# Performance work log

Hardware: AMD Instinct MI355X
Metric: run time of the kernel (lower is better)

Reference implementation:

```python
import jax, jax.numpy as jnp
import numpy as np
from functools import partial

B, N, U, E, OUT = 32, 1024, 32, 64, 64   # batch, nodes, gru units, embed dim, output dim
LIT, SEM = 12, 16                         # literal / semantic feature dims
T_FWD, L_MLP = 5, 2                       # CFGForwardTime, MLPLayer


def _gru_seq(seq, Wk, Wr, b):
    """Keras GRU (reset_after=True), return full sequence. seq: [B,T,F]."""
    b_in, b_rec = b[0], b[1]
    xproj = jnp.einsum('btf,fu->btu', seq, Wk) + b_in          # [B,T,3U]
    h0 = jnp.zeros((seq.shape[0], U), seq.dtype)

    def step(h, xt):
        rec = h @ Wr + b_rec
        xz, xr, xh = jnp.split(xt, 3, axis=-1)
        rz, rr, rh = jnp.split(rec, 3, axis=-1)
        z = jax.nn.sigmoid(xz + rz)
        r = jax.nn.sigmoid(xr + rr)
        hh = jnp.tanh(xh + r * rh)
        hn = z * h + (1.0 - z) * hh
        return hn, hn

    _, ys = jax.lax.scan(step, h0, jnp.transpose(xproj, (1, 0, 2)))
    return jnp.transpose(ys, (1, 0, 2))                         # [B,T,U]


def _data_layer(lit, sem, Win, bin_, Wout, bout, gk, grk, gb):
    mid = jax.nn.relu(lit @ Win + bin_)            # [B,N,E]
    literal = jax.nn.relu(mid @ Wout + bout)       # [B,N,32]
    semantic = _gru_seq(sem, gk, grk, gb)          # [B,N,32]
    return jnp.concatenate([literal, semantic], axis=-1)  # [B,N,64]


def _graph_layer(inp, cfg, mlpW, mlpb, wOut, bOut):
    e = jax.nn.relu(inp)
    for _ in range(T_FWD):
        t = jnp.einsum('bnm,bmd->bnd', cfg, e)     # message passing
        for i in range(L_MLP):
            t = jax.nn.relu(t @ mlpW[i] + mlpb[i])
        e = jnp.tanh(e + t)
    mid = jnp.sum(e, axis=1)                       # [B,E]
    return mid @ wOut + bOut                       # [B,OUT]


def _cosine(a, b):
    an = a / jnp.sqrt(jnp.maximum(jnp.sum(a * a, -1, keepdims=True), 1e-12))
    bn = b / jnp.sqrt(jnp.maximum(jnp.sum(b * b, -1, keepdims=True), 1e-12))
    return -jnp.sum(an * bn, -1)                   # keras cosine_similarity = -cos


def setup_inputs():
    key = jax.random.key(0)
    ks = jax.random.split(key, 32)
    g = lambda i, shp, s=0.05: jax.random.normal(ks[i], shp, jnp.float32) * s
    inp = {
        'CFG1ST': jax.random.randint(ks[0], (B, N, N), 0, 2, jnp.int32),
        'PFG1ST': jnp.zeros((1,), jnp.float32),
        'LITERAL1ST': jax.random.normal(ks[1], (B, N, LIT), jnp.float32),
        'SEMANTIC1ST': jax.random.normal(ks[2], (B, N, SEM), jnp.float32),
        'CFG2ND': jax.random.randint(ks[3], (B, N, N), 0, 2, jnp.int32),
        'PFG2ND': jnp.zeros((1,), jnp.float32),
        'LITERAL2ND': jax.random.normal(ks[4], (B, N, LIT), jnp.float32),
        'SEMANTIC2ND': jax.random.normal(ks[5], (B, N, SEM), jnp.float32),
        # data layer 1 params
        'd1_Win': g(6, (LIT, E)), 'd1_bin': jnp.zeros((E,), jnp.float32),
        'd1_Wout': g(7, (E, U)), 'd1_bout': jnp.zeros((U,), jnp.float32),
        'd1_gk': g(8, (SEM, 3 * U)), 'd1_grk': g(9, (U, 3 * U)),
        'd1_gb': jnp.zeros((2, 3 * U), jnp.float32),
        # data layer 2 params
        'd2_Win': g(10, (LIT, E)), 'd2_bin': jnp.zeros((E,), jnp.float32),
        'd2_Wout': g(11, (E, U)), 'd2_bout': jnp.zeros((U,), jnp.float32),
        'd2_gk': g(12, (SEM, 3 * U)), 'd2_grk': g(13, (U, 3 * U)),
        'd2_gb': jnp.zeros((2, 3 * U), jnp.float32),
        # shared graph layer params
        'mlpW': g(14, (L_MLP, E, E)), 'mlpb': jnp.zeros((L_MLP, E), jnp.float32),
        'wOut': g(15, (E, OUT)), 'bOut': jnp.zeros((OUT,), jnp.float32),
    }
    return inp


def reference(CFG1ST, PFG1ST, LITERAL1ST, SEMANTIC1ST, CFG2ND, PFG2ND, LITERAL2ND, SEMANTIC2ND,
              d1_Win, d1_bin, d1_Wout, d1_bout, d1_gk, d1_grk, d1_gb,
              d2_Win, d2_bin, d2_Wout, d2_bout, d2_gk, d2_grk, d2_gb,
              mlpW, mlpb, wOut, bOut):
    bb1 = _data_layer(LITERAL1ST, SEMANTIC1ST, d1_Win, d1_bin, d1_Wout, d1_bout, d1_gk, d1_grk, d1_gb)
    e1 = _graph_layer(bb1, CFG1ST.astype(jnp.float32), mlpW, mlpb, wOut, bOut)
    bb2 = _data_layer(LITERAL2ND, SEMANTIC2ND, d2_Win, d2_bin, d2_Wout, d2_bout, d2_gk, d2_grk, d2_gb)
    e2 = _graph_layer(bb2, CFG2ND.astype(jnp.float32), mlpW, mlpb, wOut, bOut)
    cosin = _cosine(e1, e2)
    label = -(cosin - 1.0) / 2.0
    return label  # [B]
```

## Files before the change

kernel.cpp:

```cpp
#include <hip/hip_runtime.h>
#include <stdint.h>
#include <math.h>

#define B_   32
#define N_   1024
#define U_   32
#define E_   64
#define LIT_ 12
#define SEM_ 16
#define GBN  64

typedef float f32x4 __attribute__((ext_vector_type(4)));
typedef short s16x8 __attribute__((ext_vector_type(8)));
#define MFMA_BF16(a,b,c) __builtin_amdgcn_mfma_f32_16x16x32_bf16(a,b,c,0,0,0)

#define F_ET0H 0ULL
#define F_ET0L 8388608ULL
#define F_ET1H 16777216ULL
#define F_ET1L 25165824ULL
#define F_EBUF 33554432ULL
#define F_CFGB 50331648ULL
#define F_WBUF 58720256ULL
#define F_MIN  58753024ULL

#define O_XPROJ 0ULL
#define O_T     25165824ULL
#define O_E     41943040ULL
#define O_OW    58720256ULL
#define O_MIN   58736640ULL

__device__ __forceinline__ float rdlane(float v, int k) {
    return __int_as_float(__builtin_amdgcn_readlane(__float_as_int(v), k));
}
__device__ __forceinline__ unsigned short bf16rne(float x) {
    unsigned u = __float_as_uint(x);
    return (unsigned short)((u + 0x7FFFu + ((u >> 16) & 1u)) >> 16);
}
__device__ __forceinline__ void hilo(float x, short& h, short& l) {
    unsigned short hb = bf16rne(x);
    float hf = __uint_as_float(((unsigned)hb) << 16);
    h = (short)hb;
    l = (short)bf16rne(x - hf);
}

__global__ __launch_bounds__(64) void k_pre(
    const float* __restrict__ lit1, const float* __restrict__ sem1,
    const float* __restrict__ lit2, const float* __restrict__ sem2,
    const float* __restrict__ Win1, const float* __restrict__ bin1,
    const float* __restrict__ Wout1, const float* __restrict__ bout1,
    const float* __restrict__ gk1, const float* __restrict__ gb1,
    const float* __restrict__ Win2, const float* __restrict__ bin2,
    const float* __restrict__ Wout2, const float* __restrict__ bout2,
    const float* __restrict__ gk2, const float* __restrict__ gb2,
    float* __restrict__ ebuf, float* __restrict__ xproj,
    const int* __restrict__ c1, const int* __restrict__ c2,
    uint8_t* __restrict__ cfgb,
    const float* __restrict__ mlpW, short* __restrict__ wbuf)
{
    const int tid = threadIdx.x;
    if (blockIdx.x >= 8192) {
        if (blockIdx.x <= 12287) {
            int g = blockIdx.x - 8192;
            long long gt = (long long)g * 64 + tid;
            #pragma unroll 4
            for (int it = 0; it < 32; ++it) {
                long long o = gt + 262144LL * it;
                const int* src = (o < 4194304LL) ? c1 : c2;
                long long oo = (o < 4194304LL) ? o : o - 4194304LL;
                const int4* p = (const int4*)(src + oo * 8);
                int4 v0 = p[0], v1 = p[1];
                unsigned bb = (unsigned)(v0.x & 1) | ((unsigned)(v0.y & 1) << 1) |
                              ((unsigned)(v0.z & 1) << 2) | ((unsigned)(v0.w & 1) << 3) |
                              ((unsigned)(v1.x & 1) << 4) | ((unsigned)(v1.y & 1) << 5) |
                              ((unsigned)(v1.z & 1) << 6) | ((unsigned)(v1.w & 1) << 7);
                cfgb[o] = (uint8_t)bb;
            }
        } else {
            for (int idx = tid; idx < 8192; idx += 64) {
                int layer = idx >> 12, rem = idx & 4095, out = rem >> 6, in = rem & 63;
                float x = mlpW[layer * 4096 + in * 64 + out];
                short h, l2; hilo(x, h, l2);
                wbuf[layer * 8192 + out * 64 + in] = h;
                wbuf[layer * 8192 + 4096 + out * 64 + in] = l2;
            }
        }
        return;
    }

    __shared__ float lit_ls[LIT_];
    __shared__ float sem_ls[SEM_];
    __shared__ float mid_ls[E_];
    const long long rowbase = (long long)blockIdx.x * 8;
    for (int rr = 0; rr < 8; ++rr) {
        long long row = rowbase + rr;
        int g = (int)(row >> 15);
        long long nIdx = row & 32767;
        const float* lit  = g ? lit2  : lit1;
        const float* sem  = g ? sem2  : sem1;
        const float* Win  = g ? Win2  : Win1;
        const float* bin  = g ? bin2  : bin1;
        const float* Wout = g ? Wout2 : Wout1;
        const float* bout = g ? bout2 : bout1;
        const float* gk   = g ? gk2   : gk1;
        const float* gbp  = g ? gb2   : gb1;

        if (tid < LIT_) lit_ls[tid] = lit[nIdx * LIT_ + tid];
        if (tid < SEM_) sem_ls[tid] = sem[nIdx * SEM_ + tid];
        __syncthreads();

        float acc = bin[tid];
        #pragma unroll
        for (int k = 0; k < LIT_; ++k) acc += lit_ls[k] * Win[k * E_ + tid];
        mid_ls[tid] = fmaxf(acc, 0.f);
        __syncthreads();

        if (tid < U_) {
            float a = bout[tid];
            #pragma unroll
            for (int k = 0; k < E_; ++k) a += mid_ls[k] * Wout[k * U_ + tid];
            ebuf[row * E_ + tid] = fmaxf(a, 0.f);
        }
        {
            float a = gbp[tid];
            #pragma unroll
            for (int k = 0; k < SEM_; ++k) a += sem_ls[k] * gk[k * 96 + tid];
            xproj[row * 96 + tid] = a;
        }
        if (tid < 32) {
            int c = 64 + tid;
            float a2 = gbp[c];
            #pragma unroll
            for (int k = 0; k < SEM_; ++k) a2 += sem_ls[k] * gk[k * 96 + c];
            xproj[row * 96 + c] = a2;
        }
        __syncthreads();
    }
}

__global__ __launch_bounds__(64) void k_gru(
    const float* __restrict__ grk1, const float* __restrict__ gb1,
    const float* __restrict__ grk2, const float* __restrict__ gb2,
    const float* __restrict__ xproj, float* __restrict__ ebuf)
{
    const int gb_i = blockIdx.x;
    const int g = gb_i >> 5;
    const float* grk = g ? grk2 : grk1;
    const float* gbp = g ? gb2 : gb1;
    const int l = threadIdx.x;
    const int j = l & 31;

    float wzr[32];
    float wh[32];
    #pragma unroll
    for (int k = 0; k < 32; ++k) {
        wzr[k] = grk[k * 96 + l];
        wh[k]  = grk[k * 96 + 64 + j];
    }
    const float brec0 = gbp[96 + l];
    const float brec1 = gbp[96 + 64 + j];

    const float* xp = xproj + (long long)gb_i * N_ * 96;
    float* eb = ebuf + (long long)gb_i * N_ * E_ + 32;

    float h = 0.f;

    auto STEP = [&](float X0, float X1, int T) {
        float a0 = brec0, a1 = 0.f, a2 = 0.f, a3 = 0.f;
        float b0 = brec1, b1 = 0.f, b2 = 0.f, b3 = 0.f;
        #pragma unroll
        for (int k = 0; k < 32; k += 4) {
            float h0 = rdlane(h, k);
            float h1 = rdlane(h, k + 1);
            float h2 = rdlane(h, k + 2);
            float h3 = rdlane(h, k + 3);
            a0 = fmaf(h0, wzr[k],     a0);  b0 = fmaf(h0, wh[k],     b0);
            a1 = fmaf(h1, wzr[k + 1], a1);  b1 = fmaf(h1, wh[k + 1], b1);
            a2 = fmaf(h2, wzr[k + 2], a2);  b2 = fmaf(h2, wh[k + 2], b2);
            a3 = fmaf(h3, wzr[k + 3], a3);  b3 = fmaf(h3, wh[k + 3], b3);
        }
        float rec0 = (a0 + a1) + (a2 + a3);
        float rec1 = (b0 + b1) + (b2 + b3);
        float s = 1.f / (1.f + __expf(-(X0 + rec0)));
        float zv = __shfl(s, j);
        float rv = __shfl(s, j + 32);
        float y  = X1 + rv * rec1;
        float e2 = __expf(2.f * y);
        float hh = 1.f - 2.f / (e2 + 1.f);
        float hn = hh + zv * (h - hh);
        h = hn;
        if (l < 32) eb[(long long)(T) * E_ + l] = fmaxf(hn, 0.f);
    };

    float x0a = xp[l],       x1a = xp[64 + j];
    float x0b = xp[96 + l],  x1b = xp[96 + 64 + j];

    for (int t = 0; t < N_; t += 2) {
        float nx0a = xp[(long long)(t + 2) * 96 + l];
        float nx1a = xp[(long long)(t + 2) * 96 + 64 + j];
        float nx0b = xp[(long long)(t + 3) * 96 + l];
        float nx1b = xp[(long long)(t + 3) * 96 + 64 + j];
        STEP(x0a, x1a, t);
        STEP(x0b, x1b, t + 1);
        x0a = nx0a; x1a = nx1a; x0b = nx0b; x1b = nx1b;
    }
}

__global__ __launch_bounds__(256) void k_etr(const float* __restrict__ ebuf,
                                             short* __restrict__ eTh)
{
    __shared__ float tls[128][68];
    const int blk = blockIdx.x, gb = blk >> 3, n0 = (blk & 7) * 128;
    const int tid = threadIdx.x;
    const float4* src = (const float4*)(ebuf + ((size_t)gb * N_ + n0) * E_);
    #pragma unroll
    for (int i = 0; i < 8; ++i) {
        int idx = tid + 256 * i;
        float4 v = src[idx];
        int row = idx >> 4, c4 = (idx & 15) << 2;
        tls[row][c4] = v.x; tls[row][c4 + 1] = v.y;
        tls[row][c4 + 2] = v.z; tls[row][c4 + 3] = v.w;
    }
    __syncthreads();
    const int w = tid >> 6, l = tid & 63;
    short* dh = eTh + ((size_t)gb << 16) + (size_t)l * 1024 + n0 + w * 32;
    #pragma unroll
    for (int ch = 0; ch < 4; ++ch) {
        s16x8 vh;
        #pragma unroll
        for (int i = 0; i < 8; ++i)
            vh[i] = (short)bf16rne(tls[w * 32 + ch * 8 + i][l]);
        *(s16x8*)(dh + ch * 8) = vh;
    }
}

template<int WET>
__global__ __launch_bounds__(256, 2) void k_msgmlp(
    const uint8_t* __restrict__ cfgb,
    const short* __restrict__ eThS, short* __restrict__ eThD,
    float* __restrict__ ebuf,
    const short* __restrict__ wbuf, const float* __restrict__ mlpb)
{
    __shared__ float tls[128][68];
    __shared__ __align__(8) unsigned lut16[32];
    __shared__ uint32_t cls[128][36];
    const int blk = blockIdx.x, gb = blk >> 3, n0 = (blk & 7) * 128;
    const int tid = threadIdx.x, w = tid >> 6, l = tid & 63;
    const int lr = l & 15, lk8 = (l >> 4) * 8;

    if (tid < 32) {
        unsigned e = tid >> 1, hf = tid & 1;
        unsigned b0 = (e >> (2 * hf)) & 1u, b1 = (e >> (2 * hf + 1)) & 1u;
        lut16[tid] = (b0 ? 0x3F80u : 0u) | (b1 ? 0x3F800000u : 0u);
    }
    {
        const uint4* srcv = (const uint4*)(cfgb + ((size_t)gb << 17) + (size_t)n0 * 128);
        #pragma unroll
        for (int i = 0; i < 4; ++i) {
            int idx = tid + 256 * i;
            uint4 v = srcv[idx];
            int base = idx * 4;
            int row = base >> 5, col = base & 31;
            *(uint4*)&cls[row][col] = v;
        }
    }
    __syncthreads();

    const short* bh = eThS + ((size_t)gb << 16) + (size_t)(w * 16 + lr) * 1024 + lk8;

    f32x4 acc[8];
    #pragma unroll
    for (int rt = 0; rt < 8; ++rt) acc[rt] = (f32x4){0.f, 0.f, 0.f, 0.f};

    #pragma unroll 2
    for (int kk = 0; kk < 1024; kk += 32) {
        s16x8 vh = *(const s16x8*)(bh + kk);
        #pragma unroll
        for (int rt = 0; rt < 8; ++rt) {
            unsigned dw = cls[rt * 16 + lr][kk >> 5];
            unsigned nb0 = (dw >> lk8) & 0xFu;
            unsigned nb1 = (dw >> (lk8 + 4)) & 0xFu;
            union { s16x8 v; unsigned long long d[2]; } A;
            A.d[0] = *(const unsigned long long*)&lut16[nb0 * 2];
            A.d[1] = *(const unsigned long long*)&lut16[nb1 * 2];
            acc[rt] = MFMA_BF16(A.v, vh, acc[rt]);
        }
    }

    #pragma unroll
    for (int rt = 0; rt < 8; ++rt)
        #pragma unroll
        for (int r = 0; r < 4; ++r)
            tls[rt * 16 + (l >> 4) * 4 + r][w * 16 + lr] = acc[rt][r];
    __syncthreads();

    float b0c[4], b1c[4];
    #pragma unroll
    for (int nt = 0; nt < 4; ++nt) {
        b0c[nt] = mlpb[nt * 16 + lr];
        b1c[nt] = mlpb[64 + nt * 16 + lr];
    }

    s16x8 ah[2][2], al[2][2];
    #pragma unroll
    for (int mt = 0; mt < 2; ++mt)
        #pragma unroll
        for (int kt = 0; kt < 2; ++kt) {
            const float* p = &tls[w * 32 + mt * 16 + lr][kt * 32 + lk8];
            #pragma unroll
            for (int i = 0; i < 8; ++i) { short hh, ll; hilo(p[i], hh, ll); ah[mt][kt][i] = hh; al[mt][kt][i] = ll; }
        }
    {
        f32x4 acc1[2][4];
        #pragma unroll
        for (int mt = 0; mt < 2; ++mt)
            #pragma unroll
            for (int nt = 0; nt < 4; ++nt)
                acc1[mt][nt] = (f32x4){b0c[nt], b0c[nt], b0c[nt], b0c[nt]};
        #pragma unroll
        for (int nt = 0; nt < 4; ++nt)
            #pragma unroll
            for (int kt = 0; kt < 2; ++kt) {
                s16x8 wth = *(const s16x8*)(wbuf + (nt * 16 + lr) * 64 + kt * 32 + lk8);
                s16x8 wtl = *(const s16x8*)(wbuf + 4096 + (nt * 16 + lr) * 64 + kt * 32 + lk8);
                #pragma unroll
                for (int mt = 0; mt < 2; ++mt) {
                    acc1[mt][nt] = MFMA_BF16(ah[mt][kt], wth, acc1[mt][nt]);
                    acc1[mt][nt] = MFMA_BF16(ah[mt][kt], wtl, acc1[mt][nt]);
                    acc1[mt][nt] = MFMA_BF16(al[mt][kt], wth, acc1[mt][nt]);
                }
            }
        #pragma unroll
        for (int mt = 0; mt < 2; ++mt)
            #pragma unroll
            for (int nt = 0; nt < 4; ++nt)
                #pragma unroll
                for (int r = 0; r < 4; ++r)
                    tls[w * 32 + mt * 16 + (l >> 4) * 4 + r][nt * 16 + lr] = fmaxf(acc1[mt][nt][r], 0.f);
    }

    #pragma unroll
    for (int mt = 0; mt < 2; ++mt)
        #pragma unroll
        for (int kt = 0; kt < 2; ++kt) {
            const float* p = &tls[w * 32 + mt * 16 + lr][kt * 32 + lk8];
            #pragma unroll
            for (int i = 0; i < 8; ++i) { short hh, ll; hilo(p[i], hh, ll); ah[mt][kt][i] = hh; al[mt][kt][i] = ll; }
        }
    f32x4 acc2[2][4];
    #pragma unroll
    for (int mt = 0; mt < 2; ++mt)
        #pragma unroll
        for (int nt = 0; nt < 4; ++nt)
            acc2[mt][nt] = (f32x4){b1c[nt], b1c[nt], b1c[nt], b1c[nt]};
    #pragma unroll
    for (int nt = 0; nt < 4; ++nt)
        #pragma unroll
        for (int kt = 0; kt < 2; ++kt) {
            s16x8 wth = *(const s16x8*)(wbuf + 8192 + (nt * 16 + lr) * 64 + kt * 32 + lk8);
            s16x8 wtl = *(const s16x8*)(wbuf + 8192 + 4096 + (nt * 16 + lr) * 64 + kt * 32 + lk8);
            #pragma unroll
            for (int mt = 0; mt < 2; ++mt) {
                acc2[mt][nt] = MFMA_BF16(ah[mt][kt], wth, acc2[mt][nt]);
                acc2[mt][nt] = MFMA_BF16(ah[mt][kt], wtl, acc2[mt][nt]);
                acc2[mt][nt] = MFMA_BF16(al[mt][kt], wth, acc2[mt][nt]);
            }
        }

    float* eb = ebuf + ((size_t)gb * N_ + n0) * E_;
    #pragma unroll
    for (int mt = 0; mt < 2; ++mt)
        #pragma unroll
        for (int nt = 0; nt < 4; ++nt)
            #pragma unroll
            for (int r = 0; r < 4; ++r) {
                int row = w * 32 + mt * 16 + (l >> 4) * 4 + r;
                int colq = nt * 16 + lr;
                float t2 = fmaxf(acc2[mt][nt][r], 0.f);
                float y = eb[(size_t)row * E_ + colq] + t2;
                float e2 = __expf(2.f * y);
                float en = 1.f - 2.f / (e2 + 1.f);
                eb[(size_t)row * E_ + colq] = en;
                if (WET) tls[row][colq] = en;
            }

    if (WET) {
        short* dh = eThD + ((size_t)gb << 16) + (size_t)l * 1024 + n0 + w * 32;
        #pragma unroll
        for (int ch = 0; ch < 4; ++ch) {
            s16x8 vh;
            #pragma unroll
            for (int i = 0; i < 8; ++i)
                vh[i] = (short)bf16rne(tls[w * 32 + ch * 8 + i][l]);
            *(s16x8*)(dh + ch * 8) = vh;
        }
    }
}

__global__ __launch_bounds__(256) void k_outp(const float* __restrict__ ebuf,
                                              float* __restrict__ part)
{
    const int gb = blockIdx.x >> 2, ch = blockIdx.x & 3;
    const int col = threadIdx.x & 63, r0 = threadIdx.x >> 6;
    const float* eb = ebuf + ((size_t)gb * N_ + ch * 256) * E_;
    float s = 0.f;
    #pragma unroll 8
    for (int i = 0; i < 64; ++i) s += eb[(size_t)(r0 + i * 4) * E_ + col];
    __shared__ float sm[4][64];
    sm[r0][col] = s;
    __syncthreads();
    if (threadIdx.x < 64)
        part[(gb * 4 + ch) * 64 + threadIdx.x] =
            sm[0][threadIdx.x] + sm[1][threadIdx.x] + sm[2][threadIdx.x] + sm[3][threadIdx.x];
}

__global__ __launch_bounds__(64) void k_fin(const float* __restrict__ part,
                                            const float* __restrict__ wOut,
                                            const float* __restrict__ bOut,
                                            float* __restrict__ dout)
{
    const int b = blockIdx.x, d = threadIdx.x;
    __shared__ float m1[64], m2[64];
    m1[d] = part[(b * 4 + 0) * 64 + d] + part[(b * 4 + 1) * 64 + d] +
            part[(b * 4 + 2) * 64 + d] + part[(b * 4 + 3) * 64 + d];
    m2[d] = part[((32 + b) * 4 + 0) * 64 + d] + part[((32 + b) * 4 + 1) * 64 + d] +
            part[((32 + b) * 4 + 2) * 64 + d] + part[((32 + b) * 4 + 3) * 64 + d];
    __syncthreads();
// ... 194 lines not shown
    }
}

extern "C" void kernel_launch(void* const* d_in, const int* in_sizes, int n_in,
                              void* d_out, int out_size, void* d_ws, size_t ws_size,
                              hipStream_t stream) {
    const int*   CFG1 = (const int*)d_in[0];
    const float* LIT1 = (const float*)d_in[2];
    const float* SEM1 = (const float*)d_in[3];
    const int*   CFG2 = (const int*)d_in[4];
    const float* LIT2 = (const float*)d_in[6];
    const float* SEM2 = (const float*)d_in[7];
    const float* d1_Win  = (const float*)d_in[8];
    const float* d1_bin  = (const float*)d_in[9];
    const float* d1_Wout = (const float*)d_in[10];
    const float* d1_bout = (const float*)d_in[11];
    const float* d1_gk   = (const float*)d_in[12];
    const float* d1_grk  = (const float*)d_in[13];
    const float* d1_gb   = (const float*)d_in[14];
    const float* d2_Win  = (const float*)d_in[15];
    const float* d2_bin  = (const float*)d_in[16];
    const float* d2_Wout = (const float*)d_in[17];
    const float* d2_bout = (const float*)d_in[18];
    const float* d2_gk   = (const float*)d_in[19];
    const float* d2_grk  = (const float*)d_in[20];
    const float* d2_gb   = (const float*)d_in[21];
    const float* mlpW = (const float*)d_in[22];
    const float* mlpb = (const float*)d_in[23];
    const float* wOut = (const float*)d_in[24];
    const float* bOut = (const float*)d_in[25];

    char* ws = (char*)d_ws;

    if (ws_size >= F_MIN) {
        float*   xproj = (float*)(ws + 0);
        short*   eT0h  = (short*)(ws + F_ET0H);
        short*   eT1h  = (short*)(ws + F_ET1H);
        float*   ebuf  = (float*)(ws + F_EBUF);
        uint8_t* cfgb  = (uint8_t*)(ws + F_CFGB);
        short*   wbuf  = (short*)(ws + F_WBUF);
        float*   part  = (float*)(ws + F_ET1L);

        k_pre<<<12289, 64, 0, stream>>>(LIT1, SEM1, LIT2, SEM2,
                                        d1_Win, d1_bin, d1_Wout, d1_bout, d1_gk, d1_gb,
                                        d2_Win, d2_bin, d2_Wout, d2_bout, d2_gk, d2_gb,
                                        ebuf, xproj, CFG1, CFG2, cfgb, mlpW, wbuf);

        k_gru<<<64, 64, 0, stream>>>(d1_grk, d1_gb, d2_grk, d2_gb, xproj, ebuf);

        k_etr<<<512, 256, 0, stream>>>(ebuf, eT0h);

        for (int it = 0; it < 5; ++it) {
            short* sh = (it & 1) ? eT1h : eT0h;
            short* dh = (it & 1) ? eT0h : eT1h;
            if (it < 4)
                k_msgmlp<1><<<512, 256, 0, stream>>>(cfgb, sh, dh, ebuf, wbuf, mlpb);
            else
                k_msgmlp<0><<<512, 256, 0, stream>>>(cfgb, sh, dh, ebuf, wbuf, mlpb);
        }

        k_outp<<<256, 256, 0, stream>>>(ebuf, part);
        k_fin<<<32, 64, 0, stream>>>(part, wOut, bOut, (float*)d_out);
    } else if (ws_size >= O_MIN) {
        float* xproj = (float*)(ws + O_XPROJ);
        float* tbuf  = (float*)(ws + O_T);
        float* ebuf  = (float*)(ws + O_E);
        float* outws = (float*)(ws + O_OW);

        k_pre<<<8192, 64, 0, stream>>>(LIT1, SEM1, LIT2, SEM2,
                                       d1_Win, d1_bin, d1_Wout, d1_bout, d1_gk, d1_gb,
                                       d2_Win, d2_bin, d2_Wout, d2_bout, d2_gk, d2_gb,
                                       ebuf, xproj, CFG1, CFG2, (uint8_t*)ws, mlpW, (short*)ws);

        k_gru<<<64, 64, 0, stream>>>(d1_grk, d1_gb, d2_grk, d2_gb, xproj, ebuf);

        for (int it = 0; it < 5; ++it) {
            k_msg_fb<<<512, 256, 0, stream>>>(CFG1, CFG2, ebuf, tbuf);
            k_mlp_fb<<<1024, 64, 0, stream>>>(tbuf, ebuf, mlpW, mlpb);
        }

        k_out<<<GBN, 64, 0, stream>>>(ebuf, wOut, bOut, outws);
        k_cos<<<32, 64, 0, stream>>>(outws, (float*)d_out);
    }
}
```

Measured before the change: 716.3 us.

## Pack two GRU sequences per wave and retile message-passing MFMA loop

The GRU kernel now runs two sequences per 64-lane wave, one per half. Each lane computes its z, r and h gate dot products directly, broadcasting h with ds_swizzle instead of readlane and dropping the cross-lane shuffle, so half as many blocks are launched. The message-passing kernel builds the 0/1 bf16 A fragment from the bitmask with bit arithmetic instead of an LDS lookup table. Each wave now covers 32 rows against all 64 feature columns, with 4 B loads per k step, and the sync after the accumulator store is removed. The serial GRU chain per lane does more FMAs per step. The removed __syncthreads may be a race unless later code is per-wave only.

```diff
diff --git a/kernel.cpp b/kernel.cpp
--- a/kernel.cpp
+++ b/kernel.cpp
@@ -15,7 +15,6 @@
 #define MFMA_BF16(a,b,c) __builtin_amdgcn_mfma_f32_16x16x32_bf16(a,b,c,0,0,0)
 
 #define F_ET0H 0ULL
-#define F_ET0L 8388608ULL
 #define F_ET1H 16777216ULL
 #define F_ET1L 25165824ULL
 #define F_EBUF 33554432ULL
@@ -29,9 +28,6 @@
 #define O_OW    58720256ULL
 #define O_MIN   58736640ULL
 
-__device__ __forceinline__ float rdlane(float v, int k) {
-    return __int_as_float(__builtin_amdgcn_readlane(__float_as_int(v), k));
-}
 __device__ __forceinline__ unsigned short bf16rne(float x) {
     unsigned u = __float_as_uint(x);
     return (unsigned short)((u + 0x7FFFu + ((u >> 16) & 1u)) >> 16);
@@ -42,6 +38,7 @@
     h = (short)hb;
     l = (short)bf16rne(x - hf);
 }
+#define SWZ(V,K) __int_as_float(__builtin_amdgcn_ds_swizzle(__float_as_int(V), ((K) << 5)))
 
 __global__ __launch_bounds__(64) void k_pre(
     const float* __restrict__ lit1, const float* __restrict__ sem1,
@@ -137,72 +134,81 @@
     }
 }
 
-__global__ __launch_bounds__(64) void k_gru(
+__global__ __launch_bounds__(64, 1) void k_gru(
     const float* __restrict__ grk1, const float* __restrict__ gb1,
     const float* __restrict__ grk2, const float* __restrict__ gb2,
     const float* __restrict__ xproj, float* __restrict__ ebuf)
 {
-    const int gb_i = blockIdx.x;
-    const int g = gb_i >> 5;
+    const int pair = blockIdx.x;
+    const int g = pair >> 4;
     const float* grk = g ? grk2 : grk1;
     const float* gbp = g ? gb2 : gb1;
     const int l = threadIdx.x;
     const int j = l & 31;
-
-    float wzr[32];
-    float wh[32];
+    const int hf = l >> 5;
+    const int seq = pair * 2 + hf;
+
+    float wz[32], wr[32], wh[32];
     #pragma unroll
     for (int k = 0; k < 32; ++k) {
-        wzr[k] = grk[k * 96 + l];
-        wh[k]  = grk[k * 96 + 64 + j];
-    }
-    const float brec0 = gbp[96 + l];
-    const float brec1 = gbp[96 + 64 + j];
-
-    const float* xp = xproj + (long long)gb_i * N_ * 96;
-    float* eb = ebuf + (long long)gb_i * N_ * E_ + 32;
+        wz[k] = grk[k * 96 + j];
+        wr[k] = grk[k * 96 + 32 + j];
+        wh[k] = grk[k * 96 + 64 + j];
+    }
+    const float bz  = gbp[96 + j];
+    const float br  = gbp[96 + 32 + j];
+    const float bhc = gbp[96 + 64 + j];
+
+    const float* xp = xproj + (size_t)seq * N_ * 96;
+    float* eb = ebuf + (size_t)seq * N_ * E_ + 32;
 
     float h = 0.f;
 
-    auto STEP = [&](float X0, float X1, int T) {
-        float a0 = brec0, a1 = 0.f, a2 = 0.f, a3 = 0.f;
-        float b0 = brec1, b1 = 0.f, b2 = 0.f, b3 = 0.f;
-        #pragma unroll
-        for (int k = 0; k < 32; k += 4) {
-            float h0 = rdlane(h, k);
-            float h1 = rdlane(h, k + 1);
-            float h2 = rdlane(h, k + 2);
-            float h3 = rdlane(h, k + 3);
-            a0 = fmaf(h0, wzr[k],     a0);  b0 = fmaf(h0, wh[k],     b0);
-            a1 = fmaf(h1, wzr[k + 1], a1);  b1 = fmaf(h1, wh[k + 1], b1);
-            a2 = fmaf(h2, wzr[k + 2], a2);  b2 = fmaf(h2, wh[k + 2], b2);
-            a3 = fmaf(h3, wzr[k + 3], a3);  b3 = fmaf(h3, wh[k + 3], b3);
-        }
-        float rec0 = (a0 + a1) + (a2 + a3);
-        float rec1 = (b0 + b1) + (b2 + b3);
-        float s = 1.f / (1.f + __expf(-(X0 + rec0)));
-        float zv = __shfl(s, j);
-        float rv = __shfl(s, j + 32);
-        float y  = X1 + rv * rec1;
+    #define DOT4(K)                                                             \
+        {                                                                       \
+            float h0 = SWZ(h, (K));                                             \
+            float h1 = SWZ(h, (K) + 1);                                         \
+            float h2 = SWZ(h, (K) + 2);                                         \
+            float h3 = SWZ(h, (K) + 3);                                         \
+            az0 = fmaf(h0, wz[(K)],     az0);  ar0 = fmaf(h0, wr[(K)],     ar0);  ah0 = fmaf(h0, wh[(K)],     ah0); \
+            az1 = fmaf(h1, wz[(K) + 1], az1);  ar1 = fmaf(h1, wr[(K) + 1], ar1);  ah1 = fmaf(h1, wh[(K) + 1], ah1); \
+            az2 = fmaf(h2, wz[(K) + 2], az2);  ar2 = fmaf(h2, wr[(K) + 2], ar2);  ah2 = fmaf(h2, wh[(K) + 2], ah2); \
+            az3 = fmaf(h3, wz[(K) + 3], az3);  ar3 = fmaf(h3, wr[(K) + 3], ar3);  ah3 = fmaf(h3, wh[(K) + 3], ah3); \
+        }
+
+    auto STEP = [&](float Xz, float Xr, float Xh, int T) {
+        float az0 = bz,  az1 = 0.f, az2 = 0.f, az3 = 0.f;
+        float ar0 = br,  ar1 = 0.f, ar2 = 0.f, ar3 = 0.f;
+        float ah0 = bhc, ah1 = 0.f, ah2 = 0.f, ah3 = 0.f;
+        DOT4(0)  DOT4(4)  DOT4(8)  DOT4(12)
+        DOT4(16) DOT4(20) DOT4(24) DOT4(28)
+        float az = (az0 + az1) + (az2 + az3);
+        float ar = (ar0 + ar1) + (ar2 + ar3);
+        float ah = (ah0 + ah1) + (ah2 + ah3);
+        float z = 1.f / (1.f + __expf(-(Xz + az)));
+        float r = 1.f / (1.f + __expf(-(Xr + ar)));
+        float y = Xh + r * ah;
         float e2 = __expf(2.f * y);
-        float hh = 1.f - 2.f / (e2 + 1.f);
-        float hn = hh + zv * (h - hh);
+        float hhv = 1.f - 2.f / (e2 + 1.f);
+        float hn = hhv + z * (h - hhv);
         h = hn;
-        if (l < 32) eb[(long long)(T) * E_ + l] = fmaxf(hn, 0.f);
+        eb[(long long)T * E_ + j] = fmaxf(hn, 0.f);
     };
 
-    float x0a = xp[l],       x1a = xp[64 + j];
-    float x0b = xp[96 + l],  x1b = xp[96 + 64 + j];
+    float xza = xp[j],      xra = xp[32 + j],      xha = xp[64 + j];
+    float xzb = xp[96 + j], xrb = xp[96 + 32 + j], xhb = xp[96 + 64 + j];
 
     for (int t = 0; t < N_; t += 2) {
-        float nx0a = xp[(long long)(t + 2) * 96 + l];
-        float nx1a = xp[(long long)(t + 2) * 96 + 64 + j];
-        float nx0b = xp[(long long)(t + 3) * 96 + l];
-        float nx1b = xp[(long long)(t + 3) * 96 + 64 + j];
-        STEP(x0a, x1a, t);
-        STEP(x0b, x1b, t + 1);
-        x0a = nx0a; x1a = nx1a; x0b = nx0b; x1b = nx1b;
-    }
+        long long o2 = (long long)(t + 2) * 96;
+        long long o3 = (long long)(t + 3) * 96;
+        float nza = xp[o2 + j], nra = xp[o2 + 32 + j], nha = xp[o2 + 64 + j];
+        float nzb = xp[o3 + j], nrb = xp[o3 + 32 + j], nhb = xp[o3 + 64 + j];
+        STEP(xza, xra, xha, t);
+        STEP(xzb, xrb, xhb, t + 1);
+        xza = nza; xra = nra; xha = nha;
+        xzb = nzb; xrb = nrb; xhb = nhb;
+    }
+    #undef DOT4
 }
 
 __global__ __launch_bounds__(256) void k_etr(const float* __restrict__ ebuf,
@@ -241,17 +247,11 @@
     const short* __restrict__ wbuf, const float* __restrict__ mlpb)
 {
     __shared__ float tls[128][68];
-    __shared__ __align__(8) unsigned lut16[32];
     __shared__ uint32_t cls[128][36];
     const int blk = blockIdx.x, gb = blk >> 3, n0 = (blk & 7) * 128;
     const int tid = threadIdx.x, w = tid >> 6, l = tid & 63;
     const int lr = l & 15, lk8 = (l >> 4) * 8;
 
-    if (tid < 32) {
-        unsigned e = tid >> 1, hf = tid & 1;
-        unsigned b0 = (e >> (2 * hf)) & 1u, b1 = (e >> (2 * hf + 1)) & 1u;
-        lut16[tid] = (b0 ? 0x3F80u : 0u) | (b1 ? 0x3F800000u : 0u);
-    }
     {
         const uint4* srcv = (const uint4*)(cfgb + ((size_t)gb << 17) + (size_t)n0 * 128);
         #pragma unroll
@@ -265,33 +265,42 @@
     }
     __syncthreads();
 
-    const short* bh = eThS + ((size_t)gb << 16) + (size_t)(w * 16 + lr) * 1024 + lk8;
-
-    f32x4 acc[8];
-    #pragma unroll
-    for (int rt = 0; rt < 8; ++rt) acc[rt] = (f32x4){0.f, 0.f, 0.f, 0.f};
+    const short* bh = eThS + ((size_t)gb << 16) + (size_t)lr * 1024 + lk8;
+
+    f32x4 acc[2][4];
+    #pragma unroll
+    for (int mt = 0; mt < 2; ++mt)
+        #pragma unroll
+        for (int nt = 0; nt < 4; ++nt)
+            acc[mt][nt] = (f32x4){0.f, 0.f, 0.f, 0.f};
 
     #pragma unroll 2
     for (int kk = 0; kk < 1024; kk += 32) {
-        s16x8 vh = *(const s16x8*)(bh + kk);
-        #pragma unroll
-        for (int rt = 0; rt < 8; ++rt) {
-            unsigned dw = cls[rt * 16 + lr][kk >> 5];
-            unsigned nb0 = (dw >> lk8) & 0xFu;
-            unsigned nb1 = (dw >> (lk8 + 4)) & 0xFu;
-            union { s16x8 v; unsigned long long d[2]; } A;
-            A.d[0] = *(const unsigned long long*)&lut16[nb0 * 2];
-            A.d[1] = *(const unsigned long long*)&lut16[nb1 * 2];
-            acc[rt] = MFMA_BF16(A.v, vh, acc[rt]);
-        }
-    }
-
-    #pragma unroll
-    for (int rt = 0; rt < 8; ++rt)
-        #pragma unroll
-        for (int r = 0; r < 4; ++r)
-            tls[rt * 16 + (l >> 4) * 4 + r][w * 16 + lr] = acc[rt][r];
-    __syncthreads();
+        s16x8 vh0 = *(const s16x8*)(bh + 0 * 16384 + kk);
+        s16x8 vh1 = *(const s16x8*)(bh + 1 * 16384 + kk);
+        s16x8 vh2 = *(const s16x8*)(bh + 2 * 16384 + kk);
+        s16x8 vh3 = *(const s16x8*)(bh + 3 * 16384 + kk);
+        #pragma unroll
+        for (int mt = 0; mt < 2; ++mt) {
+            unsigned dw = cls[w * 32 + mt * 16 + lr][kk >> 5];
+            s16x8 af;
+            #pragma unroll
+            for (int i = 0; i < 8; ++i)
+                af[i] = (short)((-(int)((dw >> (lk8 + i)) & 1u)) & 0x3F80);
+            acc[mt][0] = MFMA_BF16(af, vh0, acc[mt][0]);
+            acc[mt][1] = MFMA_BF16(af, vh1, acc[mt][1]);
+            acc[mt][2] = MFMA_BF16(af, vh2, acc[mt][2]);
+            acc[mt][3] = MFMA_BF16(af, vh3, acc[mt][3]);
+        }
+    }
+
+    #pragma unroll
+    for (int mt = 0; mt < 2; ++mt)
+        #pragma unroll
+        for (int nt = 0; nt < 4; ++nt)
+            #pragma unroll
+            for (int r = 0; r < 4; ++r)
+                tls[w * 32 + mt * 16 + (l >> 4) * 4 + r][nt * 16 + lr] = acc[mt][nt][r];
 
     float b0c[4], b1c[4];
     #pragma unroll
@@ -666,7 +675,7 @@
                                         d2_Win, d2_bin, d2_Wout, d2_bout, d2_gk, d2_gb,
                                         ebuf, xproj, CFG1, CFG2, cfgb, mlpW, wbuf);
 
-        k_gru<<<64, 64, 0, stream>>>(d1_grk, d1_gb, d2_grk, d2_gb, xproj, ebuf);
+        k_gru<<<32, 64, 0, stream>>>(d1_grk, d1_gb, d2_grk, d2_gb, xproj, ebuf);
 
         k_etr<<<512, 256, 0, stream>>>(ebuf, eT0h);
 
@@ -692,7 +701,7 @@
                                        d2_Win, d2_bin, d2_Wout, d2_bout, d2_gk, d2_gb,
                                        ebuf, xproj, CFG1, CFG2, (uint8_t*)ws, mlpW, (short*)ws);
 
-        k_gru<<<64, 64, 0, stream>>>(d1_grk, d1_gb, d2_grk, d2_gb, xproj, ebuf);
+        k_gru<<<32, 64, 0, stream>>>(d1_grk, d1_gb, d2_grk, d2_gb, xproj, ebuf);
 
         for (int it = 0; it < 5; ++it) {
             k_msg_fb<<<512, 256, 0, stream>>>(CFG1, CFG2, ebuf, tbuf);
```

New measurement: 823.4 us. +14.9%, slower.

## Store CFG adjacency as dense bf16 and feed MFMA directly from global memory

Applied to the files above, without the earlier changes.

Adds a new path, used when the workspace is large enough, that expands the int32 CFG adjacency into a dense bf16 matrix (0 or 1.0) once in the preprocessing kernel, instead of a packed bitmask. A new message/MLP kernel then loads bf16 A-fragments straight from global memory into MFMA, dropping the LDS staging and LUT bit-unpacking the bitmask kernel needed. The trade is 16x more adjacency bytes (about 128 MB) re-read on each of the five propagation steps, in exchange for simpler per-step compute. The new path only runs if the harness workspace is at least about 175 MB.

```diff
diff --git a/kernel.cpp b/kernel.cpp
--- a/kernel.cpp
+++ b/kernel.cpp
@@ -14,8 +14,15 @@
 typedef short s16x8 __attribute__((ext_vector_type(8)));
 #define MFMA_BF16(a,b,c) __builtin_amdgcn_mfma_f32_16x16x32_bf16(a,b,c,0,0,0)
 
+#define G_ET0H 0ULL
+#define G_ET1H 8388608ULL
+#define G_PART 16777216ULL
+#define G_EBUF 25165824ULL
+#define G_CFBF 41943040ULL
+#define G_WBUF 175160768ULL
+#define G_MIN  175193536ULL
+
 #define F_ET0H 0ULL
-#define F_ET0L 8388608ULL
 #define F_ET1H 16777216ULL
 #define F_ET1L 25165824ULL
 #define F_EBUF 33554432ULL
@@ -43,6 +50,7 @@
     l = (short)bf16rne(x - hf);
 }
 
+template<int PM>
 __global__ __launch_bounds__(64) void k_pre(
     const float* __restrict__ lit1, const float* __restrict__ sem1,
     const float* __restrict__ lit2, const float* __restrict__ sem2,
@@ -54,7 +62,7 @@
     const float* __restrict__ gk2, const float* __restrict__ gb2,
     float* __restrict__ ebuf, float* __restrict__ xproj,
     const int* __restrict__ c1, const int* __restrict__ c2,
-    uint8_t* __restrict__ cfgb,
+    void* __restrict__ cfgdst,
     const float* __restrict__ mlpW, short* __restrict__ wbuf)
 {
     const int tid = threadIdx.x;
@@ -69,11 +77,24 @@
                 long long oo = (o < 4194304LL) ? o : o - 4194304LL;
                 const int4* p = (const int4*)(src + oo * 8);
                 int4 v0 = p[0], v1 = p[1];
-                unsigned bb = (unsigned)(v0.x & 1) | ((unsigned)(v0.y & 1) << 1) |
-                              ((unsigned)(v0.z & 1) << 2) | ((unsigned)(v0.w & 1) << 3) |
-                              ((unsigned)(v1.x & 1) << 4) | ((unsigned)(v1.y & 1) << 5) |
-                              ((unsigned)(v1.z & 1) << 6) | ((unsigned)(v1.w & 1) << 7);
-                cfgb[o] = (uint8_t)bb;
+                if (PM == 2) {
+                    s16x8 s;
+                    s[0] = (short)((v0.x & 1) ? 0x3F80 : 0);
+                    s[1] = (short)((v0.y & 1) ? 0x3F80 : 0);
+                    s[2] = (short)((v0.z & 1) ? 0x3F80 : 0);
+                    s[3] = (short)((v0.w & 1) ? 0x3F80 : 0);
+                    s[4] = (short)((v1.x & 1) ? 0x3F80 : 0);
+                    s[5] = (short)((v1.y & 1) ? 0x3F80 : 0);
+                    s[6] = (short)((v1.z & 1) ? 0x3F80 : 0);
+                    s[7] = (short)((v1.w & 1) ? 0x3F80 : 0);
+                    ((s16x8*)cfgdst)[o] = s;
+                } else {
+                    unsigned bb = (unsigned)(v0.x & 1) | ((unsigned)(v0.y & 1) << 1) |
+                                  ((unsigned)(v0.z & 1) << 2) | ((unsigned)(v0.w & 1) << 3) |
+                                  ((unsigned)(v1.x & 1) << 4) | ((unsigned)(v1.y & 1) << 5) |
+                                  ((unsigned)(v1.z & 1) << 6) | ((unsigned)(v1.w & 1) << 7);
+                    ((uint8_t*)cfgdst)[o] = (uint8_t)bb;
+                }
             }
         } else {
             for (int idx = tid; idx < 8192; idx += 64) {
@@ -234,7 +255,158 @@
 }
 
 template<int WET>
-__global__ __launch_bounds__(256, 2) void k_msgmlp(
+__global__ __launch_bounds__(256, 2) void k_msgmlp_f(
+    const short* __restrict__ cfgbf,
+    const short* __restrict__ eThS, short* __restrict__ eThD,
+    float* __restrict__ ebuf,
+    const short* __restrict__ wbuf, const float* __restrict__ mlpb)
+{
+    __shared__ float tls[128][68];
+    const int blk = blockIdx.x, gb = blk >> 3, n0 = (blk & 7) * 128;
+    const int tid = threadIdx.x, w = tid >> 6, l = tid & 63;
+    const int lr = l & 15, lk8 = (l >> 4) * 8;
+
+    const short* bh = eThS + ((size_t)gb << 16) + (size_t)lr * 1024 + lk8;
+    const short* ap = cfgbf + ((size_t)(gb * N_ + n0 + w * 32 + lr)) * 1024 + lk8;
+
+    f32x4 acc[2][4];
+    #pragma unroll
+    for (int mt = 0; mt < 2; ++mt)
+        #pragma unroll
+        for (int nt = 0; nt < 4; ++nt)
+            acc[mt][nt] = (f32x4){0.f, 0.f, 0.f, 0.f};
+
+    #pragma unroll 2
+    for (int kk = 0; kk < 1024; kk += 32) {
+        s16x8 vh0 = *(const s16x8*)(bh + 0 * 16384 + kk);
+        s16x8 vh1 = *(const s16x8*)(bh + 1 * 16384 + kk);
+        s16x8 vh2 = *(const s16x8*)(bh + 2 * 16384 + kk);
+        s16x8 vh3 = *(const s16x8*)(bh + 3 * 16384 + kk);
+        s16x8 a0 = *(const s16x8*)(ap + 0 * 16384 + kk);
+        s16x8 a1 = *(const s16x8*)(ap + 1 * 16384 + kk);
+        acc[0][0] = MFMA_BF16(a0, vh0, acc[0][0]);
+        acc[0][1] = MFMA_BF16(a0, vh1, acc[0][1]);
+        acc[0][2] = MFMA_BF16(a0, vh2, acc[0][2]);
+        acc[0][3] = MFMA_BF16(a0, vh3, acc[0][3]);
+        acc[1][0] = MFMA_BF16(a1, vh0, acc[1][0]);
+        acc[1][1] = MFMA_BF16(a1, vh1, acc[1][1]);
+        acc[1][2] = MFMA_BF16(a1, vh2, acc[1][2]);
+        acc[1][3] = MFMA_BF16(a1, vh3, acc[1][3]);
+    }
+
+    #pragma unroll
+    for (int mt = 0; mt < 2; ++mt)
+        #pragma unroll
+        for (int nt = 0; nt < 4; ++nt)
+            #pragma unroll
+            for (int r = 0; r < 4; ++r)
+                tls[w * 32 + mt * 16 + (l >> 4) * 4 + r][nt * 16 + lr] = acc[mt][nt][r];
+
+    float b0c[4], b1c[4];
+    #pragma unroll
+    for (int nt = 0; nt < 4; ++nt) {
+        b0c[nt] = mlpb[nt * 16 + lr];
+        b1c[nt] = mlpb[64 + nt * 16 + lr];
+    }
+
+    s16x8 ah[2][2], al[2][2];
+    #pragma unroll
+    for (int mt = 0; mt < 2; ++mt)
+        #pragma unroll
+        for (int kt = 0; kt < 2; ++kt) {
+            const float* p = &tls[w * 32 + mt * 16 + lr][kt * 32 + lk8];
+            #pragma unroll
+            for (int i = 0; i < 8; ++i) { short hh, ll; hilo(p[i], hh, ll); ah[mt][kt][i] = hh; al[mt][kt][i] = ll; }
+        }
+    {
+        f32x4 acc1[2][4];
+        #pragma unroll
+        for (int mt = 0; mt < 2; ++mt)
+            #pragma unroll
+            for (int nt = 0; nt < 4; ++nt)
+                acc1[mt][nt] = (f32x4){b0c[nt], b0c[nt], b0c[nt], b0c[nt]};
+        #pragma unroll
+        for (int nt = 0; nt < 4; ++nt)
+            #pragma unroll
+            for (int kt = 0; kt < 2; ++kt) {
+                s16x8 wth = *(const s16x8*)(wbuf + (nt * 16 + lr) * 64 + kt * 32 + lk8);
+                s16x8 wtl = *(const s16x8*)(wbuf + 4096 + (nt * 16 + lr) * 64 + kt * 32 + lk8);
+                #pragma unroll
+                for (int mt = 0; mt < 2; ++mt) {
+                    acc1[mt][nt] = MFMA_BF16(ah[mt][kt], wth, acc1[mt][nt]);
+                    acc1[mt][nt] = MFMA_BF16(ah[mt][kt], wtl, acc1[mt][nt]);
+                    acc1[mt][nt] = MFMA_BF16(al[mt][kt], wth, acc1[mt][nt]);
+                }
+            }
+        #pragma unroll
+        for (int mt = 0; mt < 2; ++mt)
+            #pragma unroll
+            for (int nt = 0; nt < 4; ++nt)
+                #pragma unroll
+                for (int r = 0; r < 4; ++r)
+                    tls[w * 32 + mt * 16 + (l >> 4) * 4 + r][nt * 16 + lr] = fmaxf(acc1[mt][nt][r], 0.f);
+    }
+
+    #pragma unroll
+    for (int mt = 0; mt < 2; ++mt)
+        #pragma unroll
+        for (int kt = 0; kt < 2; ++kt) {
+            const float* p = &tls[w * 32 + mt * 16 + lr][kt * 32 + lk8];
+            #pragma unroll
+            for (int i = 0; i < 8; ++i) { short hh, ll; hilo(p[i], hh, ll); ah[mt][kt][i] = hh; al[mt][kt][i] = ll; }
+        }
+    f32x4 acc2[2][4];
+    #pragma unroll
+    for (int mt = 0; mt < 2; ++mt)
+        #pragma unroll
+        for (int nt = 0; nt < 4; ++nt)
+            acc2[mt][nt] = (f32x4){b1c[nt], b1c[nt], b1c[nt], b1c[nt]};
+    #pragma unroll
+    for (int nt = 0; nt < 4; ++nt)
+        #pragma unroll
+        for (int kt = 0; kt < 2; ++kt) {
+            s16x8 wth = *(const s16x8*)(wbuf + 8192 + (nt * 16 + lr) * 64 + kt * 32 + lk8);
+            s16x8 wtl = *(const s16x8*)(wbuf + 8192 + 4096 + (nt * 16 + lr) * 64 + kt * 32 + lk8);
+            #pragma unroll
+            for (int mt = 0; mt < 2; ++mt) {
+                acc2[mt][nt] = MFMA_BF16(ah[mt][kt], wth, acc2[mt][nt]);
+                acc2[mt][nt] = MFMA_BF16(ah[mt][kt], wtl, acc2[mt][nt]);
+                acc2[mt][nt] = MFMA_BF16(al[mt][kt], wth, acc2[mt][nt]);
+            }
+        }
+
+    float* eb = ebuf + ((size_t)gb * N_ + n0) * E_;
+    #pragma unroll
+    for (int mt = 0; mt < 2; ++mt)
+        #pragma unroll
+        for (int nt = 0; nt < 4; ++nt)
+            #pragma unroll
+            for (int r = 0; r < 4; ++r) {
+                int row = w * 32 + mt * 16 + (l >> 4) * 4 + r;
+                int colq = nt * 16 + lr;
+                float t2 = fmaxf(acc2[mt][nt][r], 0.f);
+                float y = eb[(size_t)row * E_ + colq] + t2;
+                float e2 = __expf(2.f * y);
+                float en = 1.f - 2.f / (e2 + 1.f);
+                eb[(size_t)row * E_ + colq] = en;
+                if (WET) tls[row][colq] = en;
+            }
+
+    if (WET) {
+        short* dh = eThD + ((size_t)gb << 16) + (size_t)l * 1024 + n0 + w * 32;
+        #pragma unroll
+        for (int ch = 0; ch < 4; ++ch) {
+            s16x8 vh;
+            #pragma unroll
+            for (int i = 0; i < 8; ++i)
+                vh[i] = (short)bf16rne(tls[w * 32 + ch * 8 + i][l]);
+            *(s16x8*)(dh + ch * 8) = vh;
+        }
+    }
+}
+
+template<int WET>
+__global__ __launch_bounds__(256, 2) void k_msgmlp_m(
     const uint8_t* __restrict__ cfgb,
     const short* __restrict__ eThS, short* __restrict__ eThD,
     float* __restrict__ ebuf,
@@ -652,7 +824,36 @@
 
     char* ws = (char*)d_ws;
 
-    if (ws_size >= F_MIN) {
+    if (ws_size >= G_MIN) {
+        float* xproj = (float*)(ws + 0);
+        short* eT0h  = (short*)(ws + G_ET0H);
+        short* eT1h  = (short*)(ws + G_ET1H);
+        float* part  = (float*)(ws + G_PART);
+        float* ebuf  = (float*)(ws + G_EBUF);
+        short* cfgbf = (short*)(ws + G_CFBF);
+        short* wbuf  = (short*)(ws + G_WBUF);
+
+        k_pre<2><<<12289, 64, 0, stream>>>(LIT1, SEM1, LIT2, SEM2,
+                                           d1_Win, d1_bin, d1_Wout, d1_bout, d1_gk, d1_gb,
+                                           d2_Win, d2_bin, d2_Wout, d2_bout, d2_gk, d2_gb,
+                                           ebuf, xproj, CFG1, CFG2, (void*)cfgbf, mlpW, wbuf);
+
+        k_gru<<<64, 64, 0, stream>>>(d1_grk, d1_gb, d2_grk, d2_gb, xproj, ebuf);
+
+        k_etr<<<512, 256, 0, stream>>>(ebuf, eT0h);
+
+        for (int it = 0; it < 5; ++it) {
+            short* sh = (it & 1) ? eT1h : eT0h;
+            short* dh = (it & 1) ? eT0h : eT1h;
+            if (it < 4)
+                k_msgmlp_f<1><<<512, 256, 0, stream>>>(cfgbf, sh, dh, ebuf, wbuf, mlpb);
+            else
+                k_msgmlp_f<0><<<512, 256, 0, stream>>>(cfgbf, sh, dh, ebuf, wbuf, mlpb);
+        }
+
+        k_outp<<<256, 256, 0, stream>>>(ebuf, part);
+        k_fin<<<32, 64, 0, stream>>>(part, wOut, bOut, (float*)d_out);
+    } else if (ws_size >= F_MIN) {
         float*   xproj = (float*)(ws + 0);
         short*   eT0h  = (short*)(ws + F_ET0H);
         short*   eT1h  = (short*)(ws + F_ET1H);
@@ -661,10 +862,10 @@
         short*   wbuf  = (short*)(ws + F_WBUF);
         float*   part  = (float*)(ws + F_ET1L);
 
-        k_pre<<<12289, 64, 0, stream>>>(LIT1, SEM1, LIT2, SEM2,
-                                        d1_Win, d1_bin, d1_Wout, d1_bout, d1_gk, d1_gb,
-                                        d2_Win, d2_bin, d2_Wout, d2_bout, d2_gk, d2_gb,
-                                        ebuf, xproj, CFG1, CFG2, cfgb, mlpW, wbuf);
+        k_pre<1><<<12289, 64, 0, stream>>>(LIT1, SEM1, LIT2, SEM2,
+                                           d1_Win, d1_bin, d1_Wout, d1_bout, d1_gk, d1_gb,
+                                           d2_Win, d2_bin, d2_Wout, d2_bout, d2_gk, d2_gb,
+                                           ebuf, xproj, CFG1, CFG2, (void*)cfgb, mlpW, wbuf);
 
         k_gru<<<64, 64, 0, stream>>>(d1_grk, d1_gb, d2_grk, d2_gb, xproj, ebuf);
 
@@ -674,9 +875,9 @@
             short* sh = (it & 1) ? eT1h : eT0h;
             short* dh = (it & 1) ? eT0h : eT1h;
             if (it < 4)
-                k_msgmlp<1><<<512, 256, 0, stream>>>(cfgb, sh, dh, ebuf, wbuf, mlpb);
+                k_msgmlp_m<1><<<512, 256, 0, stream>>>(cfgb, sh, dh, ebuf, wbuf, mlpb);
             else
-                k_msgmlp<0><<<512, 256, 0, stream>>>(cfgb, sh, dh, ebuf, wbuf, mlpb);
+                k_msgmlp_m<0><<<512, 256, 0, stream>>>(cfgb, sh, dh, ebuf, wbuf, mlpb);
         }
 
         k_outp<<<256, 256, 0, stream>>>(ebuf, part);
@@ -687,10 +888,10 @@
         float* ebuf  = (float*)(ws + O_E);
         float* outws = (float*)(ws + O_OW);
 
-        k_pre<<<8192, 64, 0, stream>>>(LIT1, SEM1, LIT2, SEM2,
-                                       d1_Win, d1_bin, d1_Wout, d1_bout, d1_gk, d1_gb,
-                                       d2_Win, d2_bin, d2_Wout, d2_bout, d2_gk, d2_gb,
-                                       ebuf, xproj, CFG1, CFG2, (uint8_t*)ws, mlpW, (short*)ws);
+        k_pre<1><<<8192, 64, 0, stream>>>(LIT1, SEM1, LIT2, SEM2,
+                                          d1_Win, d1_bin, d1_Wout, d1_bout, d1_gk, d1_gb,
+                                          d2_Win, d2_bin, d2_Wout, d2_bout, d2_gk, d2_gb,
+                                          ebuf, xproj, CFG1, CFG2, (void*)ws, mlpW, (short*)ws);
 
         k_gru<<<64, 64, 0, stream>>>(d1_grk, d1_gb, d2_grk, d2_gb, xproj, ebuf);
 
```

New measurement: 904.6 us. 1.26x slower.

## Retile message-passing MFMA to 2x2 wave grid and widen preprocessing blocks

Applied to the files above, without the earlier changes.

k_pre now runs 256-thread blocks with each wave handling its own 8 rows. Per-row __syncthreads and shared staging of inputs are replaced by direct global reads and per-wave shared mid buffers, and the CFG bit-packing branch is rescaled to match. In k_msgmlp the message-passing GEMM changes from each wave owning 16 columns over all 128 rows to a 2x2 wave grid (64 rows x 32 columns per wave). Each cfg A-fragment from the LUT is then reused across two B fragments, halving LUT/LDS decode work per MFMA. An extra __syncthreads is added in the MLP phase, which may add a little sync cost.

```diff
diff --git a/kernel.cpp b/kernel.cpp
--- a/kernel.cpp
+++ b/kernel.cpp
@@ -15,7 +15,6 @@
 #define MFMA_BF16(a,b,c) __builtin_amdgcn_mfma_f32_16x16x32_bf16(a,b,c,0,0,0)
 
 #define F_ET0H 0ULL
-#define F_ET0L 8388608ULL
 #define F_ET1H 16777216ULL
 #define F_ET1L 25165824ULL
 #define F_EBUF 33554432ULL
@@ -29,6 +28,8 @@
 #define O_OW    58720256ULL
 #define O_MIN   58736640ULL
 
+#define LITBLK 2048
+
 __device__ __forceinline__ float rdlane(float v, int k) {
     return __int_as_float(__builtin_amdgcn_readlane(__float_as_int(v), k));
 }
@@ -43,7 +44,7 @@
     l = (short)bf16rne(x - hf);
 }
 
-__global__ __launch_bounds__(64) void k_pre(
+__global__ __launch_bounds__(256) void k_pre(
     const float* __restrict__ lit1, const float* __restrict__ sem1,
     const float* __restrict__ lit2, const float* __restrict__ sem2,
     const float* __restrict__ Win1, const float* __restrict__ bin1,
@@ -58,13 +59,13 @@
     const float* __restrict__ mlpW, short* __restrict__ wbuf)
 {
     const int tid = threadIdx.x;
-    if (blockIdx.x >= 8192) {
-        if (blockIdx.x <= 12287) {
-            int g = blockIdx.x - 8192;
-            long long gt = (long long)g * 64 + tid;
+    if (blockIdx.x >= LITBLK) {
+        if (blockIdx.x <= LITBLK + 4095) {
+            int g = blockIdx.x - LITBLK;
+            long long gt = (long long)g * 256 + tid;
             #pragma unroll 4
-            for (int it = 0; it < 32; ++it) {
-                long long o = gt + 262144LL * it;
+            for (int it = 0; it < 8; ++it) {
+                long long o = gt + 1048576LL * it;
                 const int* src = (o < 4194304LL) ? c1 : c2;
                 long long oo = (o < 4194304LL) ? o : o - 4194304LL;
                 const int4* p = (const int4*)(src + oo * 8);
@@ -76,7 +77,7 @@
                 cfgb[o] = (uint8_t)bb;
             }
         } else {
-            for (int idx = tid; idx < 8192; idx += 64) {
+            for (int idx = tid; idx < 8192; idx += 256) {
                 int layer = idx >> 12, rem = idx & 4095, out = rem >> 6, in = rem & 63;
                 float x = mlpW[layer * 4096 + in * 64 + out];
                 short h, l2; hilo(x, h, l2);
@@ -87,12 +88,10 @@
         return;
     }
 
-    __shared__ float lit_ls[LIT_];
-    __shared__ float sem_ls[SEM_];
-    __shared__ float mid_ls[E_];
-    const long long rowbase = (long long)blockIdx.x * 8;
+    __shared__ float mid_ls[4][64];
+    const int wv = tid >> 6, lane = tid & 63;
     for (int rr = 0; rr < 8; ++rr) {
-        long long row = rowbase + rr;
+        long long row = (long long)blockIdx.x * 32 + wv * 8 + rr;
         int g = (int)(row >> 15);
         long long nIdx = row & 32767;
         const float* lit  = g ? lit2  : lit1;
@@ -104,36 +103,30 @@
         const float* gk   = g ? gk2   : gk1;
         const float* gbp  = g ? gb2   : gb1;
 
-        if (tid < LIT_) lit_ls[tid] = lit[nIdx * LIT_ + tid];
-        if (tid < SEM_) sem_ls[tid] = sem[nIdx * SEM_ + tid];
-        __syncthreads();
-
-        float acc = bin[tid];
-        #pragma unroll
-        for (int k = 0; k < LIT_; ++k) acc += lit_ls[k] * Win[k * E_ + tid];
-        mid_ls[tid] = fmaxf(acc, 0.f);
-        __syncthreads();
-
-        if (tid < U_) {
-            float a = bout[tid];
-            #pragma unroll
-            for (int k = 0; k < E_; ++k) a += mid_ls[k] * Wout[k * U_ + tid];
-            ebuf[row * E_ + tid] = fmaxf(a, 0.f);
+        float acc = bin[lane];
+        #pragma unroll
+        for (int k = 0; k < LIT_; ++k) acc += lit[nIdx * LIT_ + k] * Win[k * E_ + lane];
+        mid_ls[wv][lane] = fmaxf(acc, 0.f);
+
+        if (lane < U_) {
+            float a = bout[lane];
+            #pragma unroll 8
+            for (int k = 0; k < E_; ++k) a += mid_ls[wv][k] * Wout[k * U_ + lane];
+            ebuf[row * E_ + lane] = fmaxf(a, 0.f);
         }
         {
-            float a = gbp[tid];
-            #pragma unroll
-            for (int k = 0; k < SEM_; ++k) a += sem_ls[k] * gk[k * 96 + tid];
-            xproj[row * 96 + tid] = a;
-        }
-        if (tid < 32) {
-            int c = 64 + tid;
+            float a = gbp[lane];
+            #pragma unroll
+            for (int k = 0; k < SEM_; ++k) a += sem[nIdx * SEM_ + k] * gk[k * 96 + lane];
+            xproj[row * 96 + lane] = a;
+        }
+        if (lane < 32) {
+            int c = 64 + lane;
             float a2 = gbp[c];
             #pragma unroll
-            for (int k = 0; k < SEM_; ++k) a2 += sem_ls[k] * gk[k * 96 + c];
+            for (int k = 0; k < SEM_; ++k) a2 += sem[nIdx * SEM_ + k] * gk[k * 96 + c];
             xproj[row * 96 + c] = a2;
         }
-        __syncthreads();
     }
 }
 
@@ -246,6 +239,7 @@
     const int blk = blockIdx.x, gb = blk >> 3, n0 = (blk & 7) * 128;
     const int tid = threadIdx.x, w = tid >> 6, l = tid & 63;
     const int lr = l & 15, lk8 = (l >> 4) * 8;
+    const int rh = w & 1, ch = w >> 1;
 
     if (tid < 32) {
         unsigned e = tid >> 1, hf = tid & 1;
@@ -265,32 +259,39 @@
     }
     __syncthreads();
 
-    const short* bh = eThS + ((size_t)gb << 16) + (size_t)(w * 16 + lr) * 1024 + lk8;
-
-    f32x4 acc[8];
-    #pragma unroll
-    for (int rt = 0; rt < 8; ++rt) acc[rt] = (f32x4){0.f, 0.f, 0.f, 0.f};
+    const short* bh = eThS + ((size_t)gb << 16) + (size_t)(ch * 32 + lr) * 1024 + lk8;
+
+    f32x4 acc[4][2];
+    #pragma unroll
+    for (int rt = 0; rt < 4; ++rt)
+        #pragma unroll
+        for (int ct = 0; ct < 2; ++ct)
+            acc[rt][ct] = (f32x4){0.f, 0.f, 0.f, 0.f};
 
     #pragma unroll 2
     for (int kk = 0; kk < 1024; kk += 32) {
-        s16x8 vh = *(const s16x8*)(bh + kk);
-        #pragma unroll
-        for (int rt = 0; rt < 8; ++rt) {
-            unsigned dw = cls[rt * 16 + lr][kk >> 5];
+        s16x8 vh0 = *(const s16x8*)(bh + kk);
+        s16x8 vh1 = *(const s16x8*)(bh + 16384 + kk);
+        #pragma unroll
+        for (int rt = 0; rt < 4; ++rt) {
+            unsigned dw = cls[rh * 64 + rt * 16 + lr][kk >> 5];
             unsigned nb0 = (dw >> lk8) & 0xFu;
             unsigned nb1 = (dw >> (lk8 + 4)) & 0xFu;
             union { s16x8 v; unsigned long long d[2]; } A;
             A.d[0] = *(const unsigned long long*)&lut16[nb0 * 2];
             A.d[1] = *(const unsigned long long*)&lut16[nb1 * 2];
-            acc[rt] = MFMA_BF16(A.v, vh, acc[rt]);
-        }
-    }
-
-    #pragma unroll
-    for (int rt = 0; rt < 8; ++rt)
-        #pragma unroll
-        for (int r = 0; r < 4; ++r)
-            tls[rt * 16 + (l >> 4) * 4 + r][w * 16 + lr] = acc[rt][r];
+            acc[rt][0] = MFMA_BF16(A.v, vh0, acc[rt][0]);
+            acc[rt][1] = MFMA_BF16(A.v, vh1, acc[rt][1]);
+        }
+    }
+
+    #pragma unroll
+    for (int rt = 0; rt < 4; ++rt)
+        #pragma unroll
+        for (int ct = 0; ct < 2; ++ct)
+            #pragma unroll
+            for (int r = 0; r < 4; ++r)
+                tls[rh * 64 + rt * 16 + (l >> 4) * 4 + r][ch * 32 + ct * 16 + lr] = acc[rt][ct][r];
     __syncthreads();
 
     float b0c[4], b1c[4];
@@ -329,6 +330,7 @@
                     acc1[mt][nt] = MFMA_BF16(al[mt][kt], wth, acc1[mt][nt]);
                 }
             }
+        __syncthreads();
         #pragma unroll
         for (int mt = 0; mt < 2; ++mt)
             #pragma unroll
@@ -386,12 +388,12 @@
     if (WET) {
         short* dh = eThD + ((size_t)gb << 16) + (size_t)l * 1024 + n0 + w * 32;
         #pragma unroll
-        for (int ch = 0; ch < 4; ++ch) {
+        for (int chq = 0; chq < 4; ++chq) {
             s16x8 vh;
             #pragma unroll
             for (int i = 0; i < 8; ++i)
-                vh[i] = (short)bf16rne(tls[w * 32 + ch * 8 + i][l]);
-            *(s16x8*)(dh + ch * 8) = vh;
+                vh[i] = (short)bf16rne(tls[w * 32 + chq * 8 + i][l]);
+            *(s16x8*)(dh + chq * 8) = vh;
         }
     }
 }
@@ -661,10 +663,10 @@
         short*   wbuf  = (short*)(ws + F_WBUF);
         float*   part  = (float*)(ws + F_ET1L);
 
-        k_pre<<<12289, 64, 0, stream>>>(LIT1, SEM1, LIT2, SEM2,
-                                        d1_Win, d1_bin, d1_Wout, d1_bout, d1_gk, d1_gb,
-                                        d2_Win, d2_bin, d2_Wout, d2_bout, d2_gk, d2_gb,
-                                        ebuf, xproj, CFG1, CFG2, cfgb, mlpW, wbuf);
+        k_pre<<<LITBLK + 4097, 256, 0, stream>>>(LIT1, SEM1, LIT2, SEM2,
+                                                 d1_Win, d1_bin, d1_Wout, d1_bout, d1_gk, d1_gb,
+                                                 d2_Win, d2_bin, d2_Wout, d2_bout, d2_gk, d2_gb,
+                                                 ebuf, xproj, CFG1, CFG2, cfgb, mlpW, wbuf);
 
         k_gru<<<64, 64, 0, stream>>>(d1_grk, d1_gb, d2_grk, d2_gb, xproj, ebuf);
 
@@ -687,10 +689,10 @@
         float* ebuf  = (float*)(ws + O_E);
         float* outws = (float*)(ws + O_OW);
 
-        k_pre<<<8192, 64, 0, stream>>>(LIT1, SEM1, LIT2, SEM2,
-                                       d1_Win, d1_bin, d1_Wout, d1_bout, d1_gk, d1_gb,
-                                       d2_Win, d2_bin, d2_Wout, d2_bout, d2_gk, d2_gb,
-                                       ebuf, xproj, CFG1, CFG2, (uint8_t*)ws, mlpW, (short*)ws);
+        k_pre<<<LITBLK, 256, 0, stream>>>(LIT1, SEM1, LIT2, SEM2,
+                                          d1_Win, d1_bin, d1_Wout, d1_bout, d1_gk, d1_gb,
+                                          d2_Win, d2_bin, d2_Wout, d2_bout, d2_gk, d2_gb,
+                                          ebuf, xproj, CFG1, CFG2, (uint8_t*)ws, mlpW, (short*)ws);
 
         k_gru<<<64, 64, 0, stream>>>(d1_grk, d1_gb, d2_grk, d2_gb, xproj, ebuf);
 
```

New measurement: 650.2 us. -9.2%, faster.
